# Kernel tuning notes

Measured on AMD Instinct MI355X. Metric: run time of the kernel, lower is better.

## Reference

```python
import jax, jax.numpy as jnp
import numpy as np

# Hierarchy from the source module: super-class -> list of fine sub-classes
HIERARCHY_MAP = {0: [0, 1], 1: [2, 3, 4, 5, 6, 7, 8], 2: [9, 10, 11, 12, 13], 3: [14, 15]}
NUM_CLASSES = 16
N = 2_097_152  # batch size; logits are 128 MB fp32
EPS = 1e-8


def setup_inputs() -> dict:
    key = jax.random.key(0)
    k1, k2, k3 = jax.random.split(key, 3)
    logits = jax.random.normal(k1, (N, NUM_CLASSES), dtype=jnp.float32)
    # targets in [0, 4): valid both as fine-class indices and super-class indices
    remapped_targets = jax.random.randint(k2, (N,), 0, 4, dtype=jnp.int32)
    is_fine = jax.random.randint(k3, (N,), 0, 2, dtype=jnp.int32)  # 1 -> 'fine', 0 -> 'coarse'
    # Membership matrix M[s, c] = 1 if fine class c belongs to super class s
    mask = np.zeros((len(HIERARCHY_MAP), NUM_CLASSES), dtype=np.float32)
    for s, subs in HIERARCHY_MAP.items():
        mask[s, subs] = 1.0
    return {
        "logits": logits,
        "remapped_targets": remapped_targets,
        "is_fine": is_fine,
        "super_mask": jnp.asarray(mask),
    }


def reference(logits, remapped_targets, is_fine, super_mask):
    # log-softmax over classes, numerically stable, computed once
    log_probs = jax.nn.log_softmax(logits, axis=1)  # [N, C]
    # fine branch: -log p[target]
    fine_nll = -jnp.take_along_axis(log_probs, remapped_targets[:, None], axis=1)[:, 0]  # [N]
    # coarse branch: -log(sum_{c in subclasses(target)} p[c] + eps)
    mask_rows = super_mask[remapped_targets]  # [N, C] gather of membership rows
    coarse_nll = -jnp.log(jnp.sum(jnp.exp(log_probs) * mask_rows, axis=1) + EPS)  # [N]
    per_sample = jnp.where(is_fine == 1, fine_nll, coarse_nll)
    return jnp.mean(per_sample)
```

## Files before the change

kernel.cpp:

```cpp
#include <hip/hip_runtime.h>
#include <hip/hip_bf16.h>


#define TPB 256
#define RPT 4
#define ROWS_PER_BLOCK (TPB * RPT)

template <bool FULL>
__global__ __launch_bounds__(TPB) void hce_main(
    const float* __restrict__ logits,
    const int* __restrict__ targets,
    const int* __restrict__ is_fine,
    const float* __restrict__ super_mask,
    double* __restrict__ acc,
    int N)
{
    const int t = threadIdx.x;
    const int base = blockIdx.x * ROWS_PER_BLOCK + t;

    const float4* __restrict__ lg4 = (const float4*)logits;
    const float4* __restrict__ mk4 = (const float4*)super_mask;

    unsigned mb[4];
    #pragma unroll
    for (int s = 0; s < 4; ++s) {
        unsigned m = 0;
        #pragma unroll
        for (int q = 0; q < 4; ++q) {
            float4 v = mk4[s * 4 + q];
            m |= (v.x != 0.0f ? 1u : 0u) << (4 * q + 0);
            m |= (v.y != 0.0f ? 1u : 0u) << (4 * q + 1);
            m |= (v.z != 0.0f ? 1u : 0u) << (4 * q + 2);
            m |= (v.w != 0.0f ? 1u : 0u) << (4 * q + 3);
        }
        mb[s] = m;
    }

    float local = 0.0f;

    #pragma unroll
    for (int k = 0; k < RPT; ++k) {
        const int row = base + k * TPB;
        if (FULL || row < N) {
            float4 a = lg4[row * 4 + 0];
            float4 b = lg4[row * 4 + 1];
            float4 c = lg4[row * 4 + 2];
            float4 d = lg4[row * 4 + 3];
            const int tgt = targets[row];
            const int fin = is_fine[row];

            unsigned mcoarse = (tgt & 2) ? ((tgt & 1) ? mb[3] : mb[2])
                                         : ((tgt & 1) ? mb[1] : mb[0]);
            unsigned B = (fin == 1) ? (1u << tgt) : mcoarse;

            float e[16];
            e[0]=__expf(a.x);  e[1]=__expf(a.y);  e[2]=__expf(a.z);  e[3]=__expf(a.w);
            e[4]=__expf(b.x);  e[5]=__expf(b.y);  e[6]=__expf(b.z);  e[7]=__expf(b.w);
            e[8]=__expf(c.x);  e[9]=__expf(c.y);  e[10]=__expf(c.z); e[11]=__expf(c.w);
            e[12]=__expf(d.x); e[13]=__expf(d.y); e[14]=__expf(d.z); e[15]=__expf(d.w);

            float s = 0.0f, sel = 0.0f;
            #pragma unroll
            for (int i = 0; i < 16; ++i) {
                s += e[i];
                sel = fmaf((float)((B >> i) & 1u), e[i], sel);
            }

            local += __logf(s) - __logf(fmaf(1e-8f, s, sel));
        }
    }

    #pragma unroll
    for (int off = 1; off < 64; off <<= 1)
        local += __shfl_xor(local, off);

    __shared__ float wsum[TPB / 64];
    const int wave = t >> 6;
    if ((t & 63) == 0) wsum[wave] = local;
    __syncthreads();
    if (t == 0) {
        float blockSum = 0.0f;
        #pragma unroll
        for (int w = 0; w < TPB / 64; ++w) blockSum += wsum[w];
        atomicAdd(acc, (double)blockSum);
    }
}

__global__ void hce_finalize(const double* __restrict__ acc,
                             float* __restrict__ out, int N)
{
    out[0] = (float)(acc[0] / (double)N);
}

extern "C" void kernel_launch(void* const* d_in, const int* in_sizes, int n_in,
                              void* d_out, int out_size, void* d_ws, size_t ws_size,
                              hipStream_t stream)
{
    const float* logits     = (const float*)d_in[0];
    const int*   targets    = (const int*)d_in[1];
    const int*   is_fine    = (const int*)d_in[2];
    const float* super_mask = (const float*)d_in[3];
    float*       out        = (float*)d_out;
    double*      acc        = (double*)d_ws;

    const int N = in_sizes[1];

    hipMemsetAsync(acc, 0, sizeof(double), stream);

    const int blocks = (N + ROWS_PER_BLOCK - 1) / ROWS_PER_BLOCK;
    if (N % ROWS_PER_BLOCK == 0)
        hce_main<true><<<blocks, TPB, 0, stream>>>(logits, targets, is_fine, super_mask, acc, N);
    else
        hce_main<false><<<blocks, TPB, 0, stream>>>(logits, targets, is_fine, super_mask, acc, N);
    hce_finalize<<<1, 1, 0, stream>>>(acc, out, N);
}
```

Before: 210.0 us.

## Stage logits through padded LDS for coalesced loads and fuse finalize via ticket

Each tile of 256 rows is now loaded with fully coalesced float4 reads, where consecutive threads read consecutive 16-byte chunks, into a padded shared-memory tile. Each thread then reads its own row back from LDS, replacing the strided per-thread row loads. The separate finalize kernel is removed: the last block, detected with an atomic ticket counter, computes the mean. This adds two block barriers per tile and an LDS round trip, and removes one kernel launch.

```diff
diff --git a/kernel.cpp b/kernel.cpp
--- a/kernel.cpp
+++ b/kernel.cpp
@@ -3,8 +3,9 @@
 
 
 #define TPB 256
-#define RPT 4
-#define ROWS_PER_BLOCK (TPB * RPT)
+#define TILES 4
+#define ROWS_PER_BLOCK (TPB * TILES)
+#define LDS_ROW_STRIDE 5
 
 template <bool FULL>
 __global__ __launch_bounds__(TPB) void hce_main(
@@ -13,13 +14,15 @@
     const int* __restrict__ is_fine,
     const float* __restrict__ super_mask,
     double* __restrict__ acc,
-    int N)
+    unsigned* __restrict__ ticket,
+    float* __restrict__ out,
+    int N, int nblocks)
 {
     const int t = threadIdx.x;
-    const int base = blockIdx.x * ROWS_PER_BLOCK + t;
-
     const float4* __restrict__ lg4 = (const float4*)logits;
     const float4* __restrict__ mk4 = (const float4*)super_mask;
+
+    __shared__ float4 tile[TPB * LDS_ROW_STRIDE];
 
     unsigned mb[4];
     #pragma unroll
@@ -38,16 +41,26 @@
 
     float local = 0.0f;
 
-    #pragma unroll
-    for (int k = 0; k < RPT; ++k) {
-        const int row = base + k * TPB;
+    for (int j = 0; j < TILES; ++j) {
+        const int rowbase = blockIdx.x * ROWS_PER_BLOCK + j * TPB;
+
+        #pragma unroll
+        for (int i = 0; i < 4; ++i) {
+            const int f = i * TPB + t;
+            float4 v;
+            if (FULL || (rowbase + (f >> 2)) < N) v = lg4[rowbase * 4 + f];
+            else                                  v = make_float4(0.f, 0.f, 0.f, 0.f);
+            tile[(f >> 2) * LDS_ROW_STRIDE + (f & 3)] = v;
+        }
+
+        const int row = rowbase + t;
+        int tgt = 0, fin = 0;
+        if (FULL || row < N) { tgt = targets[row]; fin = is_fine[row]; }
+        __syncthreads();
+
         if (FULL || row < N) {
-            float4 a = lg4[row * 4 + 0];
-            float4 b = lg4[row * 4 + 1];
-            float4 c = lg4[row * 4 + 2];
-            float4 d = lg4[row * 4 + 3];
-            const int tgt = targets[row];
-            const int fin = is_fine[row];
+            const float4* r = &tile[t * LDS_ROW_STRIDE];
+            float4 a = r[0], b = r[1], c = r[2], d = r[3];
 
             unsigned mcoarse = (tgt & 2) ? ((tgt & 1) ? mb[3] : mb[2])
                                          : ((tgt & 1) ? mb[1] : mb[0]);
@@ -65,9 +78,10 @@
                 s += e[i];
                 sel = fmaf((float)((B >> i) & 1u), e[i], sel);
             }
-
             local += __logf(s) - __logf(fmaf(1e-8f, s, sel));
         }
+
+        if (j < TILES - 1) __syncthreads();
     }
 
     #pragma unroll
@@ -83,13 +97,13 @@
         #pragma unroll
         for (int w = 0; w < TPB / 64; ++w) blockSum += wsum[w];
         atomicAdd(acc, (double)blockSum);
+        __threadfence();
+        unsigned old = atomicAdd(ticket, 1u);
+        if (old == (unsigned)(nblocks - 1)) {
+            double total = atomicAdd(acc, 0.0);
+            out[0] = (float)(total / (double)N);
+        }
     }
-}
-
-__global__ void hce_finalize(const double* __restrict__ acc,
-                             float* __restrict__ out, int N)
-{
-    out[0] = (float)(acc[0] / (double)N);
 }
 
 extern "C" void kernel_launch(void* const* d_in, const int* in_sizes, int n_in,
@@ -102,15 +116,17 @@
     const float* super_mask = (const float*)d_in[3];
     float*       out        = (float*)d_out;
     double*      acc        = (double*)d_ws;
+    unsigned*    ticket     = (unsigned*)((char*)d_ws + 8);
 
     const int N = in_sizes[1];
 
-    hipMemsetAsync(acc, 0, sizeof(double), stream);
+    hipMemsetAsync(d_ws, 0, 16, stream);
 
     const int blocks = (N + ROWS_PER_BLOCK - 1) / ROWS_PER_BLOCK;
     if (N % ROWS_PER_BLOCK == 0)
-        hce_main<true><<<blocks, TPB, 0, stream>>>(logits, targets, is_fine, super_mask, acc, N);
+        hce_main<true><<<blocks, TPB, 0, stream>>>(logits, targets, is_fine, super_mask,
+                                                   acc, ticket, out, N, blocks);
     else
-        hce_main<false><<<blocks, TPB, 0, stream>>>(logits, targets, is_fine, super_mask, acc, N);
-    hce_finalize<<<1, 1, 0, stream>>>(acc, out, N);
+        hce_main<false><<<blocks, TPB, 0, stream>>>(logits, targets, is_fine, super_mask,
+                                                    acc, ticket, out, N, blocks);
 }
```

After: 303.4 us. 44.5% more time.
